# Optimization experiments

Measured on AMD Instinct MI355X. Metric: run time of the kernel, lower is better.

## Reference

```python
import jax, jax.numpy as jnp
import numpy as np

N = 100000
E = 1600000
NFEAT = 128
NHID = 16
HEADS = 4
NCLASS = 40
NEG_SLOPE = 0.2
BN_EPS = 1e-5


def setup_inputs() -> dict:
    key = jax.random.key(0)
    ks = jax.random.split(key, 16)
    HC = NHID * HEADS  # 64
    x = jax.random.normal(ks[0], (N, NFEAT), dtype=jnp.float32)
    edge_index = jax.random.randint(ks[1], (2, E), 0, N, dtype=jnp.int64)
    def glorot(k, shape, fan_in):
        return jax.random.normal(k, shape, dtype=jnp.float32) * (1.0 / np.sqrt(fan_in))
    return {
        "x": x,
        "edge_index": edge_index,
        # layer 1: GATConv(NFEAT -> NHID, heads=HEADS, concat=True)
        "W1": glorot(ks[2], (NFEAT, HC), NFEAT),
        "att_src1": glorot(ks[3], (HEADS, NHID), NHID),
        "att_dst1": glorot(ks[4], (HEADS, NHID), NHID),
        "bias1": jnp.zeros((HC,), dtype=jnp.float32),
        # BatchNorm1d(HC), eval mode (running stats)
        "bn_gamma": jnp.ones((HC,), dtype=jnp.float32),
        "bn_beta": jnp.zeros((HC,), dtype=jnp.float32),
        "bn_mean": jax.random.normal(ks[5], (HC,), dtype=jnp.float32) * 0.1,
        "bn_var": jax.random.uniform(ks[6], (HC,), dtype=jnp.float32, minval=0.5, maxval=1.5),
        # layer 2: GATConv(HC -> NCLASS, heads=1, concat=False)
        "W2": glorot(ks[7], (HC, NCLASS), HC),
        "att_src2": glorot(ks[8], (1, NCLASS), NCLASS),
        "att_dst2": glorot(ks[9], (1, NCLASS), NCLASS),
        "bias2": jnp.zeros((NCLASS,), dtype=jnp.float32),
    }


def gat_conv(x, src, dst, W, att_src, att_dst, bias, concat):
    """PyG GATConv (eval; self-loops assumed already appended to src/dst)."""
    H, C = att_src.shape
    n = x.shape[0]
    h = (x @ W).reshape(n, H, C)                         # [N,H,C]
    a_s = (h * att_src[None]).sum(-1)                    # [N,H]
    a_d = (h * att_dst[None]).sum(-1)                    # [N,H]
    alpha = jax.nn.leaky_relu(a_s[src] + a_d[dst], NEG_SLOPE)  # [Et,H]
    # segment softmax over incoming edges of each destination node
    amax = jax.ops.segment_max(alpha, dst, num_segments=n)    # [N,H]
    ex = jnp.exp(alpha - amax[dst])
    denom = jax.ops.segment_sum(ex, dst, num_segments=n)
    coef = ex / denom[dst]                               # [Et,H]
    msg = h[src] * coef[:, :, None]                      # [Et,H,C]
    out = jax.ops.segment_sum(msg, dst, num_segments=n)  # [N,H,C]
    out = out.reshape(n, H * C) if concat else out.mean(axis=1)
    return out + bias


def reference(x, edge_index, W1, att_src1, att_dst1, bias1,
              bn_gamma, bn_beta, bn_mean, bn_var,
              W2, att_src2, att_dst2, bias2):
    n = x.shape[0]
    loops = jnp.arange(n, dtype=edge_index.dtype)
    src = jnp.concatenate([edge_index[0], loops])
    dst = jnp.concatenate([edge_index[1], loops])
    h = gat_conv(x, src, dst, W1, att_src1, att_dst1, bias1, concat=True)
    h = (h - bn_mean) * jax.lax.rsqrt(bn_var + BN_EPS) * bn_gamma + bn_beta
    h = jax.nn.relu(h)  # dropout is identity in eval
    out = gat_conv(h, src, dst, W2, att_src2, att_dst2, bias2, concat=False)
    return out
```

## Files before the change

### kernel.cpp

```cpp
#include <hip/hip_runtime.h>
#include <hip/hip_bf16.h>
#include <hip/hip_fp16.h>

#define NFEAT  128
#define HC     64
#define HEADS  4
#define NHID   16
#define NCLASS 40
#define NEG    0.2f
#define BN_EPS 1e-5f

#define BK_SH   9
#define CHUNK   8192
#define STAGE   12288

typedef _Float16 half8_t __attribute__((ext_vector_type(8)));
typedef _Float16 half4_t __attribute__((ext_vector_type(4)));
typedef float    f32x4_t __attribute__((ext_vector_type(4)));

__device__ __forceinline__ float leaky(float a) { return (a > 0.f) ? a : NEG * a; }

__global__ __launch_bounds__(256) void k_gemm1(
    const float* __restrict__ x, const float* __restrict__ W1,
    const float* __restrict__ att_s, const float* __restrict__ att_d,
    __half* __restrict__ h1, float* __restrict__ as1, float* __restrict__ ad1,
    int n)
{
    const int wave = threadIdx.x >> 6, lane = threadIdx.x & 63;
    const int quad = lane >> 4, l16 = lane & 15;

    half8_t bfrag[4][4];
    #pragma unroll
    for (int ks = 0; ks < 4; ++ks)
        #pragma unroll
        for (int ct = 0; ct < 4; ++ct)
            #pragma unroll
            for (int j = 0; j < 8; ++j)
                bfrag[ks][ct][j] =
                    (_Float16)W1[(ks * 32 + quad * 8 + j) * HC + ct * 16 + l16];

    float avs[4], avd[4];
    #pragma unroll
    for (int ct = 0; ct < 4; ++ct) {
        avs[ct] = att_s[ct * 16 + l16];
        avd[ct] = att_d[ct * 16 + l16];
    }

    const int nslab = (n + 15) >> 4;
    for (int slab = blockIdx.x * 4 + wave; slab < nslab; slab += gridDim.x * 4) {
        const int rowbase = slab * 16;
        const int arow = min(rowbase + l16, n - 1);
        const float* xp = x + (size_t)arow * NFEAT;

        f32x4_t acc[4] = {{0.f,0.f,0.f,0.f},{0.f,0.f,0.f,0.f},
                          {0.f,0.f,0.f,0.f},{0.f,0.f,0.f,0.f}};
        #pragma unroll
        for (int ks = 0; ks < 4; ++ks) {
            const float4 xa = *(const float4*)(xp + ks * 32 + quad * 8);
            const float4 xb = *(const float4*)(xp + ks * 32 + quad * 8 + 4);
            half8_t af;
            af[0] = (_Float16)xa.x; af[1] = (_Float16)xa.y;
            af[2] = (_Float16)xa.z; af[3] = (_Float16)xa.w;
            af[4] = (_Float16)xb.x; af[5] = (_Float16)xb.y;
            af[6] = (_Float16)xb.z; af[7] = (_Float16)xb.w;
            #pragma unroll
            for (int ct = 0; ct < 4; ++ct)
                acc[ct] = __builtin_amdgcn_mfma_f32_16x16x32_f16(
                    af, bfrag[ks][ct], acc[ct], 0, 0, 0);
        }

        #pragma unroll
        for (int reg = 0; reg < 4; ++reg) {
            const int row = rowbase + quad * 4 + reg;
            const bool valid = row < n;

            float4 ps, pd;
            ps.x = acc[0][reg] * avs[0]; pd.x = acc[0][reg] * avd[0];
            ps.y = acc[1][reg] * avs[1]; pd.y = acc[1][reg] * avd[1];
            ps.z = acc[2][reg] * avs[2]; pd.z = acc[2][reg] * avd[2];
            ps.w = acc[3][reg] * avs[3]; pd.w = acc[3][reg] * avd[3];
            #pragma unroll
            for (int off = 8; off >= 1; off >>= 1) {
                ps.x += __shfl_xor(ps.x, off, 64); pd.x += __shfl_xor(pd.x, off, 64);
                ps.y += __shfl_xor(ps.y, off, 64); pd.y += __shfl_xor(pd.y, off, 64);
                ps.z += __shfl_xor(ps.z, off, 64); pd.z += __shfl_xor(pd.z, off, 64);
                ps.w += __shfl_xor(ps.w, off, 64); pd.w += __shfl_xor(pd.w, off, 64);
            }
            if (valid) {
                #pragma unroll
                for (int ct = 0; ct < 4; ++ct)
                    h1[(size_t)row * HC + ct * 16 + l16] =
                        __float2half_rn(acc[ct][reg]);
                if (l16 == 0) {
                    *(float4*)(as1 + (size_t)row * HEADS) = ps;
                    *(float4*)(ad1 + (size_t)row * HEADS) = pd;
                }
            }
        }
    }
}

__global__ __launch_bounds__(512) void k_hist(
    const int* __restrict__ edst, int* __restrict__ hist, int E, int nbk)
{
    __shared__ int lh[256];
    const int w = blockIdx.x, t = threadIdx.x;
    for (int i = t; i < nbk; i += 512) lh[i] = 0;
    __syncthreads();
    const int lo = w * CHUNK, hi = min(E, lo + CHUNK);
    for (int e = lo + 4 * t; e < hi; e += 4 * 512) {
        const int4 d4 = *(const int4*)(edst + e);
        atomicAdd(&lh[d4.x >> BK_SH], 1);
        atomicAdd(&lh[d4.y >> BK_SH], 1);
        atomicAdd(&lh[d4.z >> BK_SH], 1);
        atomicAdd(&lh[d4.w >> BK_SH], 1);
    }
    __syncthreads();
    for (int i = t; i < nbk; i += 512) hist[(size_t)w * nbk + i] = lh[i];
}

__global__ __launch_bounds__(256) void k_colscan(
    int* __restrict__ hist, int* __restrict__ colsum, int nbk, int nw)
{
    __shared__ int wred[4];
    const int b = blockIdx.x, t = threadIdx.x;
    const int lane = t & 63, w = t >> 6;
    const int v = (t < nw) ? hist[(size_t)t * nbk + b] : 0;
    int sc = v;
    #pragma unroll
    for (int off = 1; off < 64; off <<= 1) {
        int u = __shfl_up(sc, off, 64);
        if (lane >= off) sc += u;
    }
    if (lane == 63) wred[w] = sc;
    __syncthreads();
    if (t == 0) { int a = 0; for (int i = 0; i < 4; ++i) { int xx = wred[i]; wred[i] = a; a += xx; } }
    __syncthreads();
    const int excl = sc - v + wred[w];
    if (t < nw) hist[(size_t)t * nbk + b] = excl;
    if (t == nw - 1) colsum[b] = excl + v;
}

__global__ __launch_bounds__(256) void k_bscan(
    const int* __restrict__ colsum, int* __restrict__ bstart, int nbk, int E)
{
    __shared__ int wred[4];
    const int t = threadIdx.x, lane = t & 63, w = t >> 6;
    const int v = (t < nbk) ? colsum[t] : 0;
    int sc = v;
    #pragma unroll
    for (int off = 1; off < 64; off <<= 1) {
        int u = __shfl_up(sc, off, 64);
        if (lane >= off) sc += u;
    }
    if (lane == 63) wred[w] = sc;
    __syncthreads();
    if (t == 0) { int a = 0; for (int i = 0; i < 4; ++i) { int xx = wred[i]; wred[i] = a; a += xx; } }
    __syncthreads();
    if (t < nbk) bstart[t] = sc - v + wred[w];
    if (t == 0) bstart[nbk] = E;
}

__global__ __launch_bounds__(512) void k_scatter(
    const int* __restrict__ esrc, const int* __restrict__ edst,
    const int* __restrict__ hist, const int* __restrict__ bstart,
    int2* __restrict__ pairs, int E, int nbk)
{
    __shared__ int cur[256];
    const int w = blockIdx.x, t = threadIdx.x;
    for (int i = t; i < nbk; i += 512)
        cur[i] = bstart[i] + hist[(size_t)w * nbk + i];
    __syncthreads();
    const int lo = w * CHUNK, hi = min(E, lo + CHUNK);
    for (int e = lo + 4 * t; e < hi; e += 4 * 512) {
        const int4 s4 = *(const int4*)(esrc + e);
        const int4 d4 = *(const int4*)(edst + e);
        int pos;
        pos = atomicAdd(&cur[d4.x >> BK_SH], 1); pairs[pos] = make_int2(s4.x, d4.x);
        pos = atomicAdd(&cur[d4.y >> BK_SH], 1); pairs[pos] = make_int2(s4.y, d4.y);
        pos = atomicAdd(&cur[d4.z >> BK_SH], 1); pairs[pos] = make_int2(s4.z, d4.z);
        pos = atomicAdd(&cur[d4.w >> BK_SH], 1); pairs[pos] = make_int2(s4.w, d4.w);
    }
}

__global__ __launch_bounds__(512) void k_build(
    const int2* __restrict__ pairs, const int* __restrict__ bstart,
    int* __restrict__ rowptr, int* __restrict__ csr, int n, int nbk)
{
    __shared__ int cnt[512];
    __shared__ int cur[512];
    __shared__ int stage[STAGE];
    __shared__ int wred[8];
    const int b = blockIdx.x, t = threadIdx.x;
    const int base = bstart[b], eend = bstart[b + 1], m = eend - base;
    const int n0 = b << BK_SH;
    const int nn = min(512, n - n0);

    cnt[t] = 0;
    __syncthreads();
    for (int e = base + t; e < eend; e += 512)
        atomicAdd(&cnt[pairs[e].y - n0], 1);
    __syncthreads();

    const int v = cnt[t];
    const int lane = t & 63, w = t >> 6;
    int sc = v;
    #pragma unroll
    for (int off = 1; off < 64; off <<= 1) {
        int u = __shfl_up(sc, off, 64);
        if (lane >= off) sc += u;
    }
    if (lane == 63) wred[w] = sc;
    __syncthreads();
    if (t == 0) { int a = 0; for (int i = 0; i < 8; ++i) { int xx = wred[i]; wred[i] = a; a += xx; } }
    __syncthreads();
    const int excl = sc - v + wred[w];
    cur[t] = excl;
    if (t < nn) rowptr[n0 + t] = base + excl + v;
    __syncthreads();

    for (int e = base + t; e < eend; e += 512) {
        const int2 p = pairs[e];
        const int loc = atomicAdd(&cur[p.y - n0], 1);
        if (loc < STAGE) stage[loc] = p.x;
        else             csr[base + loc] = p.x;
    }
    __syncthreads();
    const int lim = min(m, STAGE);
    for (int i = t; i < lim; i += 512) csr[base + i] = stage[i];
}

__global__ __launch_bounds__(256) void k_agg1(
    const int* __restrict__ csr, const int* __restrict__ rowptr,
    const __half* __restrict__ h1, const float* __restrict__ as1,
    const float* __restrict__ ad1,
    const float* __restrict__ bias1, const float* __restrict__ gamma,
    const float* __restrict__ beta, const float* __restrict__ mean,
    const float* __restrict__ var,
    const float* __restrict__ W2, const float* __restrict__ ats2,
    const float* __restrict__ atd2,
    __half* __restrict__ g, float* __restrict__ as2o, float* __restrict__ ad2o,
    int n)
{
    __shared__ _Float16 sWh[NCLASS * HC];
    __shared__ float sh[16][68];
    __shared__ float sE[16][132];
    __shared__ int   sS[16][33];
    for (int i = threadIdx.x; i < NCLASS * HC; i += 256) sWh[i] = (_Float16)W2[i];
    __syncthreads();

    const int gi = threadIdx.x >> 4;
    const int q  = threadIdx.x & 15;
    const int myh = q >> 2;

    const float4 b1v = *(const float4*)(bias1 + 4 * q);
    const float4 gmv = *(const float4*)(gamma + 4 * q);
    const float4 vrv = *(const float4*)(var   + 4 * q);
    const float4 mnv = *(const float4*)(mean  + 4 * q);
    const float4 btv = *(const float4*)(beta  + 4 * q);
    float4 scv, shv;
    scv.x = gmv.x * rsqrtf(vrv.x + BN_EPS);
    scv.y = gmv.y * rsqrtf(vrv.y + BN_EPS);
    scv.z = gmv.z * rsqrtf(vrv.z + BN_EPS);
    scv.w = gmv.w * rsqrtf(vrv.w + BN_EPS);
    shv.x = btv.x - mnv.x * scv.x;
    shv.y = btv.y - mnv.y * scv.y;
    shv.z = btv.z - mnv.z * scv.z;
    shv.w = btv.w - mnv.w * scv.w;
    float4 at2 = {0.f, 0.f, 0.f, 0.f}, dt2 = {0.f, 0.f, 0.f, 0.f};
    if (q < 10) {
        at2 = *(const float4*)(ats2 + 4 * q);
        dt2 = *(const float4*)(atd2 + 4 * q);
    }

    for (int node0 = blockIdx.x * 16; node0 < n; node0 += gridDim.x * 16) {
        const int node = node0 + gi;
        if (node >= n) continue;

        const float4 adv = *(const float4*)(ad1 + node * HEADS);
        const float4 sv4 = *(const float4*)(as1 + node * HEADS);
        float4 eself;
        eself.x = __expf(leaky(sv4.x + adv.x));
        eself.y = __expf(leaky(sv4.y + adv.y));
        eself.z = __expf(leaky(sv4.z + adv.z));
        eself.w = __expf(leaky(sv4.w + adv.w));
        const float es = (myh == 0) ? eself.x : (myh == 1) ? eself.y
                       : (myh == 2) ? eself.z : eself.w;

        float2 raws = *(const float2*)(h1 + (size_t)node * HC + 4 * q);
        const float2 s0v = __half22float2(*(__half2*)&raws.x);
        const float2 s1v = __half22float2(*(__half2*)&raws.y);
        float4 acc;
        acc.x = es * s0v.x; acc.y = es * s0v.y;
        acc.z = es * s1v.x; acc.w = es * s1v.y;
        float4 dpart = {0.f, 0.f, 0.f, 0.f};

        const int start = (node == 0) ? 0 : rowptr[node - 1];
        const int end   = rowptr[node];

        for (int base = start; base < end; base += 32) {
            const int m = min(32, end - base);
            float4 ea = {0.f, 0.f, 0.f, 0.f}, eb = {0.f, 0.f, 0.f, 0.f};
            int ia = 0, ib = 0;
            if (q < m) {
                ia = csr[base + q];
                const float4 s4 = *(const float4*)(as1 + (size_t)ia * HEADS);
                ea.x = __expf(leaky(s4.x + adv.x));
                ea.y = __expf(leaky(s4.y + adv.y));
                ea.z = __expf(leaky(s4.z + adv.z));
                ea.w = __expf(leaky(s4.w + adv.w));
            }
            if (q + 16 < m) {
                ib = csr[base + q + 16];
                const float4 s4 = *(const float4*)(as1 + (size_t)ib * HEADS);
                eb.x = __expf(leaky(s4.x + adv.x));
                eb.y = __expf(leaky(s4.y + adv.y));
                eb.z = __expf(leaky(s4.z + adv.z));
                eb.w = __expf(leaky(s4.w + adv.w));
            }
            dpart.x += ea.x + eb.x; dpart.y += ea.y + eb.y;
            dpart.z += ea.z + eb.z; dpart.w += ea.w + eb.w;
            *(float4*)&sE[gi][4 * q] = ea;
            *(float4*)&sE[gi][4 * (q + 16)] = eb;
            sS[gi][q] = ia; sS[gi][q + 16] = ib;
            __threadfence_block();

            const int*   sB = &sS[gi][0];
            const float* eB = &sE[gi][0];
            int j = 0;
            const int sa0 = sB[0];
            const int sa1 = sB[(m > 1) ? 1 : 0];
            float2 w0 = *(const float2*)(h1 + (size_t)sa0 * HC + 4 * q);
            float2 w1 = *(const float2*)(h1 + (size_t)sa1 * HC + 4 * q);
            for (; j + 2 < m; j += 2) {
                const int sn0 = sB[j + 2];
                const int sn1 = sB[(j + 3 < m) ? (j + 3) : (j + 2)];
                const float2 v0 = *(const float2*)(h1 + (size_t)sn0 * HC + 4 * q);
                const float2 v1 = *(const float2*)(h1 + (size_t)sn1 * HC + 4 * q);
                const float e0 = eB[(j + 0) * 4 + myh];
                const float e1 = eB[(j + 1) * 4 + myh];
                const float2 a0 = __half22float2(*(const __half2*)&w0.x);
                const float2 a1 = __half22float2(*(const __half2*)&w0.y);
                const float2 b0 = __half22float2(*(const __half2*)&w1.x);
                const float2 b1 = __half22float2(*(const __half2*)&w1.y);
                acc.x = fmaf(e0, a0.x, acc.x); acc.y = fmaf(e0, a0.y, acc.y);
                acc.z = fmaf(e0, a1.x, acc.z); acc.w = fmaf(e0, a1.y, acc.w);
                acc.x = fmaf(e1, b0.x, acc.x); acc.y = fmaf(e1, b0.y, acc.y);
                acc.z = fmaf(e1, b1.x, acc.z); acc.w = fmaf(e1, b1.y, acc.w);
                w0 = v0; w1 = v1;
            }
            {
                const float e0 = eB[j * 4 + myh];
                const float e1 = (j + 1 < m) ? eB[(j + 1) * 4 + myh] : 0.f;
                const float2 a0 = __half22float2(*(const __half2*)&w0.x);
                const float2 a1 = __half22float2(*(const __half2*)&w0.y);
                const float2 b0 = __half22float2(*(const __half2*)&w1.x);
                const float2 b1 = __half22float2(*(const __half2*)&w1.y);
                acc.x = fmaf(e0, a0.x, acc.x); acc.y = fmaf(e0, a0.y, acc.y);
                acc.z = fmaf(e0, a1.x, acc.z); acc.w = fmaf(e0, a1.y, acc.w);
                acc.x = fmaf(e1, b0.x, acc.x); acc.y = fmaf(e1, b0.y, acc.y);
                acc.z = fmaf(e1, b1.x, acc.z); acc.w = fmaf(e1, b1.y, acc.w);
            }
            __threadfence_block();
        }

        #pragma unroll
        for (int off = 8; off >= 1; off >>= 1) {
            dpart.x += __shfl_xor(dpart.x, off, 64);
            dpart.y += __shfl_xor(dpart.y, off, 64);
            dpart.z += __shfl_xor(dpart.z, off, 64);
            dpart.w += __shfl_xor(dpart.w, off, 64);
        }
        const float den = es + ((myh == 0) ? dpart.x : (myh == 1) ? dpart.y
                               : (myh == 2) ? dpart.z : dpart.w);
        const float rden = 1.f / den;

        float4 v;
        v.x = fmaxf(fmaf(acc.x * rden + b1v.x, scv.x, shv.x), 0.f);
        v.y = fmaxf(fmaf(acc.y * rden + b1v.y, scv.y, shv.y), 0.f);
        v.z = fmaxf(fmaf(acc.z * rden + b1v.z, scv.z, shv.z), 0.f);
        v.w = fmaxf(fmaf(acc.w * rden + b1v.w, scv.w, shv.w), 0.f);
        *(float4*)&sh[gi][4 * q] = v;
        __threadfence_block();

        float4 gacc = {0.f, 0.f, 0.f, 0.f};
        if (q < 10) {
            #pragma unroll 8
            for (int k = 0; k < HC; ++k) {
                const float hk = sh[gi][k];
                const half4_t wv = *(const half4_t*)&sWh[k * NCLASS + 4 * q];
                gacc.x = fmaf(hk, (float)wv[0], gacc.x);
                gacc.y = fmaf(hk, (float)wv[1], gacc.y);
                gacc.z = fmaf(hk, (float)wv[2], gacc.z);
                gacc.w = fmaf(hk, (float)wv[3], gacc.w);
            }
        }
        __half2 p0 = __float22half2_rn({gacc.x, gacc.y});
        __half2 p1 = __float22half2_rn({gacc.z, gacc.w});
        float2 packed; *(__half2*)&packed.x = p0; *(__half2*)&packed.y = p1;
        *(float2*)(g + (size_t)node * HC + 4 * q) = packed;

        float sv = gacc.x * at2.x + gacc.y * at2.y + gacc.z * at2.z + gacc.w * at2.w;
        float dv = gacc.x * dt2.x + gacc.y * dt2.y + gacc.z * dt2.z + gacc.w * dt2.w;
        #pragma unroll
        for (int off = 8; off >= 1; off >>= 1) {
            sv += __shfl_xor(sv, off, 64);
            dv += __shfl_xor(dv, off, 64);
        }
        if (q == 0) { as2o[node] = sv; ad2o[node] = dv; }
        __threadfence_block();
    }
}

__global__ __launch_bounds__(256) void k_agg2(
    const int* __restrict__ csr, const int* __restrict__ rowptr,
    const __half* __restrict__ g, const float* __restrict__ as2,
    const float* __restrict__ ad2, const float* __restrict__ bias2,
    float* __restrict__ out, int n)
{
    __shared__ float sE[16][34];
    __shared__ int   sS[16][33];
    const int gi = threadIdx.x >> 4;
    const int q  = threadIdx.x & 15;

    float4 b2v = {0.f, 0.f, 0.f, 0.f};
    if (q < 10) b2v = *(const float4*)(bias2 + 4 * q);

    for (int node0 = blockIdx.x * 16; node0 < n; node0 += gridDim.x * 16) {
        const int node = node0 + gi;
        if (node >= n) continue;

        const float ad2d = ad2[node];
        const float eself = __expf(leaky(as2[node] + ad2d));

        float2 raws = *(const float2*)(g + (size_t)node * HC + 4 * q);
        const float2 s0v = __half22float2(*(__half2*)&raws.x);
        const float2 s1v = __half22float2(*(__half2*)&raws.y);
        float4 acc;
        acc.x = eself * s0v.x; acc.y = eself * s0v.y;
        acc.z = eself * s1v.x; acc.w = eself * s1v.y;
        float dpart = 0.f;

        const int start = (node == 0) ? 0 : rowptr[node - 1];
        const int end   = rowptr[node];

        for (int base = start; base < end; base += 32) {
            const int m = min(32, end - base);
            float ea = 0.f, eb = 0.f;
            int ia = 0, ib = 0;
            if (q < m) {
                ia = csr[base + q];
                ea = __expf(leaky(as2[ia] + ad2d));
            }
            if (q + 16 < m) {
                ib = csr[base + q + 16];
                eb = __expf(leaky(as2[ib] + ad2d));
            }
            dpart += ea + eb;
            sE[gi][q] = ea; sE[gi][q + 16] = eb;
            sS[gi][q] = ia; sS[gi][q + 16] = ib;
            __threadfence_block();

            const int*   sB = &sS[gi][0];
            const float* eB = &sE[gi][0];
            int j = 0;
            const int sa0 = sB[0];
            const int sa1 = sB[(m > 1) ? 1 : 0];
            float2 w0 = *(const float2*)(g + (size_t)sa0 * HC + 4 * q);
            float2 w1 = *(const float2*)(g + (size_t)sa1 * HC + 4 * q);
            for (; j + 2 < m; j += 2) {
                const int sn0 = sB[j + 2];
                const int sn1 = sB[(j + 3 < m) ? (j + 3) : (j + 2)];
                const float2 v0 = *(const float2*)(g + (size_t)sn0 * HC + 4 * q);
                const float2 v1 = *(const float2*)(g + (size_t)sn1 * HC + 4 * q);
                const float e0 = eB[j + 0];
                const float e1 = eB[j + 1];
                const float2 a0 = __half22float2(*(const __half2*)&w0.x);
                const float2 a1 = __half22float2(*(const __half2*)&w0.y);
                const float2 b0 = __half22float2(*(const __half2*)&w1.x);
                const float2 b1 = __half22float2(*(const __half2*)&w1.y);
                acc.x = fmaf(e0, a0.x, acc.x); acc.y = fmaf(e0, a0.y, acc.y);
                acc.z = fmaf(e0, a1.x, acc.z); acc.w = fmaf(e0, a1.y, acc.w);
                acc.x = fmaf(e1, b0.x, acc.x); acc.y = fmaf(e1, b0.y, acc.y);
                acc.z = fmaf(e1, b1.x, acc.z); acc.w = fmaf(e1, b1.y, acc.w);
                w0 = v0; w1 = v1;
            }
            {
                const float e0 = eB[j];
                const float e1 = (j + 1 < m) ? eB[j + 1] : 0.f;
                const float2 a0 = __half22float2(*(const __half2*)&w0.x);
                const float2 a1 = __half22float2(*(const __half2*)&w0.y);
                const float2 b0 = __half22float2(*(const __half2*)&w1.x);
                const float2 b1 = __half22float2(*(const __half2*)&w1.y);
                acc.x = fmaf(e0, a0.x, acc.x); acc.y = fmaf(e0, a0.y, acc.y);
                acc.z = fmaf(e0, a1.x, acc.z); acc.w = fmaf(e0, a1.y, acc.w);
                acc.x = fmaf(e1, b0.x, acc.x); acc.y = fmaf(e1, b0.y, acc.y);
                acc.z = fmaf(e1, b1.x, acc.z); acc.w = fmaf(e1, b1.y, acc.w);
            }
            __threadfence_block();
        }

        #pragma unroll
        for (int off = 8; off >= 1; off >>= 1)
            dpart += __shfl_xor(dpart, off, 64);
        const float rden = 1.f / (dpart + eself);

        if (q < 10) {
            float4 r;
            r.x = acc.x * rden + b2v.x;
            r.y = acc.y * rden + b2v.y;
            r.z = acc.z * rden + b2v.z;
            r.w = acc.w * rden + b2v.w;
            *(float4*)(out + (size_t)node * NCLASS + 4 * q) = r;
        }
    }
}

extern "C" void kernel_launch(void* const* d_in, const int* in_sizes, int n_in,
                              void* d_out, int out_size, void* d_ws, size_t ws_size,
                              hipStream_t stream)
{
    const float* x    = (const float*)d_in[0];
    const int*   ei   = (const int*)  d_in[1];
    const float* W1   = (const float*)d_in[2];
    const float* as1w = (const float*)d_in[3];
    const float* ad1w = (const float*)d_in[4];
    const float* b1   = (const float*)d_in[5];
    const float* gm   = (const float*)d_in[6];
    const float* bt   = (const float*)d_in[7];
    const float* mn   = (const float*)d_in[8];
    const float* vr   = (const float*)d_in[9];
    const float* W2   = (const float*)d_in[10];
    const float* as2w = (const float*)d_in[11];
    const float* ad2w = (const float*)d_in[12];
    const float* b2   = (const float*)d_in[13];

    const int n = in_sizes[0] / NFEAT;
    const int E = in_sizes[1] / 2;
    const int* esrc = ei;
    const int* edst = ei + E;

    const int nbk = (n + 511) >> BK_SH;
    const int nw  = (E + CHUNK - 1) / CHUNK;

    float*  ws   = (float*)d_ws;
    __half* h1   = (__half*)ws;
    float*  a_s1 = ws   + (size_t)n * 32;
    float*  a_d1 = a_s1 + (size_t)n * 4;
    __half* gbuf = (__half*)(a_d1 + (size_t)n * 4);
    float*  a_s2 = a_d1 + (size_t)n * 4 + (size_t)n * 32;
    float*  a_d2 = a_s2 + n;
    int2*   pairs  = (int2*)(a_d2 + n);
    int*    csr    = (int*)(pairs + E);
    int*    rowptr = csr + E;
    int*    hist   = rowptr + n;
    int*    colsum = hist + (size_t)nw * nbk;
    int*    bstart = colsum + nbk;
    float*  outv = (float*)d_out;

    const int nblk = (n + 15) / 16;

    k_hist   <<<nw, 512, 0, stream>>>(edst, hist, E, nbk);
    k_colscan<<<nbk, 256, 0, stream>>>(hist, colsum, nbk, nw);
    k_bscan  <<<1, 256, 0, stream>>>(colsum, bstart, nbk, E);
    k_scatter<<<nw, 512, 0, stream>>>(esrc, edst, hist, bstart, pairs, E, nbk);
    k_build  <<<nbk, 512, 0, stream>>>(pairs, bstart, rowptr, csr, n, nbk);
    k_gemm1  <<<512, 256, 0, stream>>>(x, W1, as1w, ad1w, h1, a_s1, a_d1, n);
    k_agg1   <<<nblk, 256, 0, stream>>>(csr, rowptr, h1, a_s1, a_d1,
                                        b1, gm, bt, mn, vr,
                                        W2, as2w, ad2w, gbuf, a_s2, a_d2, n);
    k_agg2   <<<nblk, 256, 0, stream>>>(csr, rowptr, gbuf, a_s2, a_d2,
                                        b2, outv, n);
}
```

Measured before the change: 275.6 us.

## Issue all neighbor feature gathers up front via shuffles in aggregation kernels

Both aggregation kernels now process neighbors in chunks of 16 instead of 32. Neighbor indices are broadcast with wavefront shuffles instead of being staged in shared memory, and all 16 feature-row gathers are issued into a register array before the accumulation loop. The aim is more memory-level parallelism than the old two-deep software prefetch, and removing the index shared-memory traffic. Launch bounds also request 4 blocks per CU. This raises register pressure and adds more loop iterations for high-degree nodes.

Result: slower. 323.0 us (+17.2%).

```diff
diff --git a/kernel.cpp b/kernel.cpp
--- a/kernel.cpp
+++ b/kernel.cpp
@@ -230,7 +230,7 @@
     for (int i = t; i < lim; i += 512) csr[base + i] = stage[i];
 }
 
-__global__ __launch_bounds__(256) void k_agg1(
+__global__ __launch_bounds__(256, 4) void k_agg1(
     const int* __restrict__ csr, const int* __restrict__ rowptr,
     const __half* __restrict__ h1, const float* __restrict__ as1,
     const float* __restrict__ ad1,
@@ -244,14 +244,14 @@
 {
     __shared__ _Float16 sWh[NCLASS * HC];
     __shared__ float sh[16][68];
-    __shared__ float sE[16][132];
-    __shared__ int   sS[16][33];
+    __shared__ float sE[16][68];
     for (int i = threadIdx.x; i < NCLASS * HC; i += 256) sWh[i] = (_Float16)W2[i];
     __syncthreads();
 
     const int gi = threadIdx.x >> 4;
     const int q  = threadIdx.x & 15;
     const int myh = q >> 2;
+    const int gbase = threadIdx.x & 48;
 
     const float4 b1v = *(const float4*)(bias1 + 4 * q);
     const float4 gmv = *(const float4*)(gamma + 4 * q);
@@ -298,68 +298,44 @@
         const int start = (node == 0) ? 0 : rowptr[node - 1];
         const int end   = rowptr[node];
 
-        for (int base = start; base < end; base += 32) {
-            const int m = min(32, end - base);
-            float4 ea = {0.f, 0.f, 0.f, 0.f}, eb = {0.f, 0.f, 0.f, 0.f};
-            int ia = 0, ib = 0;
+        for (int base = start; base < end; base += 16) {
+            const int m = min(16, end - base);
+            int ia = 0;
+            if (q < m) ia = csr[base + q];
+
+            float4 s4 = {0.f, 0.f, 0.f, 0.f};
+            if (q < m) s4 = *(const float4*)(as1 + (size_t)ia * HEADS);
+
+            float2 wreg[16];
+            #pragma unroll
+            for (int e = 0; e < 16; ++e) {
+                if (e < m) {
+                    const int idx = __shfl(ia, gbase + e, 64);
+                    wreg[e] = *(const float2*)(h1 + (size_t)idx * HC + 4 * q);
+                }
+            }
+
+            float4 ea = {0.f, 0.f, 0.f, 0.f};
             if (q < m) {
-                ia = csr[base + q];
-                const float4 s4 = *(const float4*)(as1 + (size_t)ia * HEADS);
                 ea.x = __expf(leaky(s4.x + adv.x));
                 ea.y = __expf(leaky(s4.y + adv.y));
                 ea.z = __expf(leaky(s4.z + adv.z));
                 ea.w = __expf(leaky(s4.w + adv.w));
             }
-            if (q + 16 < m) {
-                ib = csr[base + q + 16];
-                const float4 s4 = *(const float4*)(as1 + (size_t)ib * HEADS);
-                eb.x = __expf(leaky(s4.x + adv.x));
-                eb.y = __expf(leaky(s4.y + adv.y));
-                eb.z = __expf(leaky(s4.z + adv.z));
-                eb.w = __expf(leaky(s4.w + adv.w));
-            }
-            dpart.x += ea.x + eb.x; dpart.y += ea.y + eb.y;
-            dpart.z += ea.z + eb.z; dpart.w += ea.w + eb.w;
+            dpart.x += ea.x; dpart.y += ea.y;
+            dpart.z += ea.z; dpart.w += ea.w;
             *(float4*)&sE[gi][4 * q] = ea;
-            *(float4*)&sE[gi][4 * (q + 16)] = eb;
-            sS[gi][q] = ia; sS[gi][q + 16] = ib;
             __threadfence_block();
 
-            const int*   sB = &sS[gi][0];
-            const float* eB = &sE[gi][0];
-            int j = 0;
-            const int sa0 = sB[0];
-            const int sa1 = sB[(m > 1) ? 1 : 0];
-            float2 w0 = *(const float2*)(h1 + (size_t)sa0 * HC + 4 * q);
-            float2 w1 = *(const float2*)(h1 + (size_t)sa1 * HC + 4 * q);
-            for (; j + 2 < m; j += 2) {
-                const int sn0 = sB[j + 2];
-                const int sn1 = sB[(j + 3 < m) ? (j + 3) : (j + 2)];
-                const float2 v0 = *(const float2*)(h1 + (size_t)sn0 * HC + 4 * q);
-                const float2 v1 = *(const float2*)(h1 + (size_t)sn1 * HC + 4 * q);
-                const float e0 = eB[(j + 0) * 4 + myh];
-                const float e1 = eB[(j + 1) * 4 + myh];
-                const float2 a0 = __half22float2(*(const __half2*)&w0.x);
-                const float2 a1 = __half22float2(*(const __half2*)&w0.y);
-                const float2 b0 = __half22float2(*(const __half2*)&w1.x);
-                const float2 b1 = __half22float2(*(const __half2*)&w1.y);
-                acc.x = fmaf(e0, a0.x, acc.x); acc.y = fmaf(e0, a0.y, acc.y);
-                acc.z = fmaf(e0, a1.x, acc.z); acc.w = fmaf(e0, a1.y, acc.w);
-                acc.x = fmaf(e1, b0.x, acc.x); acc.y = fmaf(e1, b0.y, acc.y);
-                acc.z = fmaf(e1, b1.x, acc.z); acc.w = fmaf(e1, b1.y, acc.w);
-                w0 = v0; w1 = v1;
-            }
-            {
-                const float e0 = eB[j * 4 + myh];
-                const float e1 = (j + 1 < m) ? eB[(j + 1) * 4 + myh] : 0.f;
-                const float2 a0 = __half22float2(*(const __half2*)&w0.x);
-                const float2 a1 = __half22float2(*(const __half2*)&w0.y);
-                const float2 b0 = __half22float2(*(const __half2*)&w1.x);
-                const float2 b1 = __half22float2(*(const __half2*)&w1.y);
-                acc.x = fmaf(e0, a0.x, acc.x); acc.y = fmaf(e0, a0.y, acc.y);
-                acc.z = fmaf(e0, a1.x, acc.z); acc.w = fmaf(e0, a1.y, acc.w);
-                acc.x = fmaf(e1, b0.x, acc.x); acc.y = fmaf(e1, b0.y, acc.y);
-                acc.z = fmaf(e1, b1.x, acc.z); acc.w = fmaf(e1, b1.y, acc.w);
+            #pragma unroll
+            for (int e = 0; e < 16; ++e) {
+                if (e < m) {
+                    const float ee = sE[gi][4 * e + myh];
+                    const float2 a0 = __half22float2(*(const __half2*)&wreg[e].x);
+                    const float2 a1 = __half22float2(*(const __half2*)&wreg[e].y);
+                    acc.x = fmaf(ee, a0.x, acc.x); acc.y = fmaf(ee, a0.y, acc.y);
+                    acc.z = fmaf(ee, a1.x, acc.z); acc.w = fmaf(ee, a1.y, acc.w);
+                }
             }
             __threadfence_block();
         }
@@ -412,16 +388,16 @@
     }
 }
 
-__global__ __launch_bounds__(256) void k_agg2(
+__global__ __launch_bounds__(256, 4) void k_agg2(
     const int* __restrict__ csr, const int* __restrict__ rowptr,
     const __half* __restrict__ g, const float* __restrict__ as2,
     const float* __restrict__ ad2, const float* __restrict__ bias2,
     float* __restrict__ out, int n)
 {
-    __shared__ float sE[16][34];
-    __shared__ int   sS[16][33];
+    __shared__ float sE[16][17];
     const int gi = threadIdx.x >> 4;
     const int q  = threadIdx.x & 15;
+    const int gbase = threadIdx.x & 48;
 
     float4 b2v = {0.f, 0.f, 0.f, 0.f};
     if (q < 10) b2v = *(const float4*)(bias2 + 4 * q);
@@ -444,58 +420,38 @@
         const int start = (node == 0) ? 0 : rowptr[node - 1];
         const int end   = rowptr[node];
 
-        for (int base = start; base < end; base += 32) {
-            const int m = min(32, end - base);
-            float ea = 0.f, eb = 0.f;
-            int ia = 0, ib = 0;
-            if (q < m) {
-                ia = csr[base + q];
-                ea = __expf(leaky(as2[ia] + ad2d));
-            }
-            if (q + 16 < m) {
-                ib = csr[base + q + 16];
-                eb = __expf(leaky(as2[ib] + ad2d));
-            }
-            dpart += ea + eb;
-            sE[gi][q] = ea; sE[gi][q + 16] = eb;
-            sS[gi][q] = ia; sS[gi][q + 16] = ib;
+        for (int base = start; base < end; base += 16) {
+            const int m = min(16, end - base);
+            int ia = 0;
+            if (q < m) ia = csr[base + q];
+
+            float sca = 0.f;
+            if (q < m) sca = as2[ia];
+
+            float2 wreg[16];
+            #pragma unroll
+            for (int e = 0; e < 16; ++e) {
+                if (e < m) {
+                    const int idx = __shfl(ia, gbase + e, 64);
+                    wreg[e] = *(const float2*)(g + (size_t)idx * HC + 4 * q);
+                }
+            }
+
+            float ea = 0.f;
+            if (q < m) ea = __expf(leaky(sca + ad2d));
+            dpart += ea;
+            sE[gi][q] = ea;
             __threadfence_block();
 
-            const int*   sB = &sS[gi][0];
-            const float* eB = &sE[gi][0];
-            int j = 0;
-            const int sa0 = sB[0];
-            const int sa1 = sB[(m > 1) ? 1 : 0];
-            float2 w0 = *(const float2*)(g + (size_t)sa0 * HC + 4 * q);
-            float2 w1 = *(const float2*)(g + (size_t)sa1 * HC + 4 * q);
-            for (; j + 2 < m; j += 2) {
-                const int sn0 = sB[j + 2];
-                const int sn1 = sB[(j + 3 < m) ? (j + 3) : (j + 2)];
-                const float2 v0 = *(const float2*)(g + (size_t)sn0 * HC + 4 * q);
-                const float2 v1 = *(const float2*)(g + (size_t)sn1 * HC + 4 * q);
-                const float e0 = eB[j + 0];
-                const float e1 = eB[j + 1];
-                const float2 a0 = __half22float2(*(const __half2*)&w0.x);
-                const float2 a1 = __half22float2(*(const __half2*)&w0.y);
-                const float2 b0 = __half22float2(*(const __half2*)&w1.x);
-                const float2 b1 = __half22float2(*(const __half2*)&w1.y);
-                acc.x = fmaf(e0, a0.x, acc.x); acc.y = fmaf(e0, a0.y, acc.y);
-                acc.z = fmaf(e0, a1.x, acc.z); acc.w = fmaf(e0, a1.y, acc.w);
-                acc.x = fmaf(e1, b0.x, acc.x); acc.y = fmaf(e1, b0.y, acc.y);
-                acc.z = fmaf(e1, b1.x, acc.z); acc.w = fmaf(e1, b1.y, acc.w);
-                w0 = v0; w1 = v1;
-            }
-            {
-                const float e0 = eB[j];
-                const float e1 = (j + 1 < m) ? eB[j + 1] : 0.f;
-                const float2 a0 = __half22float2(*(const __half2*)&w0.x);
-                const float2 a1 = __half22float2(*(const __half2*)&w0.y);
-                const float2 b0 = __half22float2(*(const __half2*)&w1.x);
-                const float2 b1 = __half22float2(*(const __half2*)&w1.y);
-                acc.x = fmaf(e0, a0.x, acc.x); acc.y = fmaf(e0, a0.y, acc.y);
-                acc.z = fmaf(e0, a1.x, acc.z); acc.w = fmaf(e0, a1.y, acc.w);
-                acc.x = fmaf(e1, b0.x, acc.x); acc.y = fmaf(e1, b0.y, acc.y);
-                acc.z = fmaf(e1, b1.x, acc.z); acc.w = fmaf(e1, b1.y, acc.w);
+            #pragma unroll
+            for (int e = 0; e < 16; ++e) {
+                if (e < m) {
+                    const float ee = sE[gi][e];
+                    const float2 a0 = __half22float2(*(const __half2*)&wreg[e].x);
+                    const float2 a1 = __half22float2(*(const __half2*)&wreg[e].y);
+                    acc.x = fmaf(ee, a0.x, acc.x); acc.y = fmaf(ee, a0.y, acc.y);
+                    acc.z = fmaf(ee, a1.x, acc.z); acc.w = fmaf(ee, a1.y, acc.w);
+                }
             }
             __threadfence_block();
         }
```
